# Kernel tuning notes

Hardware: AMD Instinct MI355X
Metric: run time of the kernel (lower is better)

## Reference

```python
import jax, jax.numpy as jnp
import numpy as np

OUT = 4096       # out_features
IN = 4096        # in_features
GS = 128         # group_size
G = IN // GS     # num_groups = 32 (IN divisible by GS -> no padding path)


def setup_inputs() -> dict:
    key = jax.random.key(0)
    k1, k2, k3 = jax.random.split(key, 3)
    x = jax.random.normal(k1, (4096, IN), dtype=jnp.float32)
    # packed int4 weights: each byte holds two 4-bit codes in [0,15] (offset-8)
    qweight = jax.random.randint(k2, (OUT, IN // 2), 0, 256, dtype=jnp.int32)
    # per-(row, group) positive scales
    scale = jax.random.uniform(k3, (OUT, G, 1), dtype=jnp.float32,
                               minval=0.01, maxval=0.1)
    return {"x": x, "qweight": qweight, "scale": scale}


def reference(x, qweight, scale):
    # unpack_int4: high nibble is the even-position element, low nibble odd
    high = (qweight >> 4) & 15
    low = qweight & 15
    q = jnp.stack([high, low], axis=-1).reshape(OUT, -1)  # [OUT, IN]
    q = q.astype(jnp.float32) - 8.0                       # back to [-8, 7]
    # group-wise dequantization
    w = q.reshape(OUT, G, GS) * scale                     # [OUT, G, GS]
    B = x.shape[0]
    xg = x.reshape(B, G, GS)                              # [B, G, GS]
    return jnp.einsum('bgs,ogs->bo', xg, w)               # [B, OUT]
```

## Files before the change

### kernel.cpp

```cpp
#include <hip/hip_runtime.h>

typedef __attribute__((ext_vector_type(8))) _Float16 f16x8;
typedef __attribute__((ext_vector_type(4))) float    f32x4;
typedef __attribute__((ext_vector_type(4))) int      i32x4;

#define IN_F   4096
#define OUT_F  4096
#define NGRP   32
#define NKT    64

#define GLOAD16(gsrc, ldst)                                                   \
    __builtin_amdgcn_global_load_lds(                                         \
        (const __attribute__((address_space(1))) unsigned int*)(gsrc),        \
        (__attribute__((address_space(3))) unsigned int*)(ldst), 16, 0, 0)

#define CFENCE  asm volatile("" ::: "memory")
#define BARRIER do { CFENCE; __builtin_amdgcn_s_barrier(); CFENCE; } while (0)
#define VMW2    asm volatile("s_waitcnt vmcnt(2)" ::: "memory")

__global__ __launch_bounds__(256)
void cvt_x(const float* __restrict__ X, _Float16* __restrict__ Y) {
    size_t i = ((size_t)blockIdx.x * 256 + threadIdx.x) * 8;
    f32x4 a = *(const f32x4*)(X + i);
    f32x4 b = *(const f32x4*)(X + i + 4);
    f16x8 h;
    h[0] = (_Float16)a[0]; h[1] = (_Float16)a[1];
    h[2] = (_Float16)a[2]; h[3] = (_Float16)a[3];
    h[4] = (_Float16)b[0]; h[5] = (_Float16)b[1];
    h[6] = (_Float16)b[2]; h[7] = (_Float16)b[3];
    *(f16x8*)(Y + i) = h;
}

__global__ __launch_bounds__(256)
void deq_w(const int* __restrict__ QW, const float* __restrict__ S,
           _Float16* __restrict__ W) {
    size_t t  = (size_t)blockIdx.x * 256 + threadIdx.x;
    size_t jj = t * 4;
    size_t o  = jj >> 11;
    size_t jr = jj & 2047;
    const float s = S[o * NGRP + (jr >> 6)];
    i32x4 q = *(const i32x4*)(QW + jj);
    f16x8 h;
#pragma unroll
    for (int j = 0; j < 4; ++j) {
        const int v = q[j];
        h[2 * j]     = (_Float16)((float)(((v >> 4) & 15) - 8) * s);
        h[2 * j + 1] = (_Float16)((float)((v & 15) - 8) * s);
    }
    *(f16x8*)(W + jj * 2) = h;
}

__global__ __launch_bounds__(512, 2)
void gemm8p(const _Float16* __restrict__ A,
            const _Float16* __restrict__ B,
            float*          __restrict__ C)
{
    extern __shared__ char LDSc[];
    char* const ldsA = LDSc;
    char* const ldsB = LDSc + 65536;

    const int tid  = threadIdx.x;
    const int lane = tid & 63;
    const int wid  = tid >> 6;
    const int wm   = wid >> 2;
    const int wn   = wid & 3;

    const int bid = blockIdx.x;
    const int swz = (bid & 7) * 32 + (bid >> 3);
    const int bm0 = (swz >> 4) * 256;
    const int bn0 = (swz & 15) * 256;

    const int r0 = tid >> 3;
    const int cs = ((tid & 7) * 16) ^ ((r0 & 7) << 4);
    const _Float16* Asrc = A + (size_t)(bm0 + r0) * IN_F + (cs >> 1);
    const _Float16* Bsrc = B + (size_t)(bn0 + r0) * IN_F + (cs >> 1);
    const int dstoff = wid * 1024;

    const int lane15 = lane & 15;
    const int swr = (lane & 7) << 4;
    const int c0 = ((lane >> 4) * 16) ^ swr;
    const int c1 = (64 + (lane >> 4) * 16) ^ swr;
    int rAoff[4], rBoff[2];
#pragma unroll
    for (int mm = 0; mm < 4; ++mm) rAoff[mm] = (wm * 64 + mm * 16 + lane15) * 128;
#pragma unroll
    for (int nn = 0; nn < 2; ++nn) rBoff[nn] = (wn * 32 + nn * 16 + lane15) * 128;

    f16x8 afr[4][2], blo[2][2], bhi[2][2];
    f32x4 acc[8][4];
#pragma unroll
    for (int m = 0; m < 8; ++m)
#pragma unroll
        for (int n = 0; n < 4; ++n) acc[m][n] = (f32x4)0.0f;

#define STAGE_A(HALF, KT, BUF) do {                                           \
        const _Float16* s_ = Asrc + (size_t)(HALF) * 128 * IN_F + (KT) * 64;  \
        char* d_ = ldsA + ((BUF) * 2 + (HALF)) * 16384 + dstoff;              \
        GLOAD16(s_, d_);                                                      \
        GLOAD16(s_ + (size_t)64 * IN_F, d_ + 8192); } while (0)

#define STAGE_B(HALF, KT, BUF) do {                                           \
        const _Float16* s_ = Bsrc + (size_t)(HALF) * 128 * IN_F + (KT) * 64;  \
        char* d_ = ldsB + ((BUF) * 2 + (HALF)) * 16384 + dstoff;              \
        GLOAD16(s_, d_);                                                      \
        GLOAD16(s_ + (size_t)64 * IN_F, d_ + 8192); } while (0)

#define RD_A(BUF, QM) do { char* ab_ = ldsA + ((BUF) * 2 + (QM)) * 16384;     \
        _Pragma("unroll") for (int mm = 0; mm < 4; ++mm) {                    \
            afr[mm][0] = *(const f16x8*)(ab_ + rAoff[mm] + c0);               \
            afr[mm][1] = *(const f16x8*)(ab_ + rAoff[mm] + c1); } } while (0)

#define RD_B(BUF, QN, DST) do { char* bb_ = ldsB + ((BUF) * 2 + (QN)) * 16384;\
        _Pragma("unroll") for (int nn = 0; nn < 2; ++nn) {                    \
            DST[nn][0] = *(const f16x8*)(bb_ + rBoff[nn] + c0);               \
            DST[nn][1] = *(const f16x8*)(bb_ + rBoff[nn] + c1); } } while (0)

#define MFMA_Q(QM, QN, BQ)                                                    \
        __builtin_amdgcn_s_setprio(1);                                        \
        _Pragma("unroll") for (int mm = 0; mm < 4; ++mm)                      \
        _Pragma("unroll") for (int nn = 0; nn < 2; ++nn)                      \
        _Pragma("unroll") for (int kk = 0; kk < 2; ++kk)                      \
            acc[(QM)*4+mm][(QN)*2+nn] =                                       \
                __builtin_amdgcn_mfma_f32_16x16x32_f16(                       \
                    afr[mm][kk], BQ[nn][kk], acc[(QM)*4+mm][(QN)*2+nn],0,0,0);\
        __builtin_amdgcn_s_setprio(0);

#define GROUP(BUF, NX) do {                                                   \
                                                           \
        VMW2; RD_A(BUF, 0); RD_B(BUF, 0, blo); STAGE_A(0, NX, (BUF) ^ 1);     \
        BARRIER; MFMA_Q(0, 0, blo); BARRIER;                                  \
                                                           \
        VMW2; RD_B(BUF, 1, bhi); STAGE_B(0, NX, (BUF) ^ 1);                   \
        BARRIER; MFMA_Q(0, 1, bhi); BARRIER;                                  \
                                                           \
        RD_A(BUF, 1); STAGE_B(1, NX, (BUF) ^ 1);                              \
        BARRIER; MFMA_Q(1, 0, blo); BARRIER;                                  \
                                                           \
        VMW2; STAGE_A(1, NX, (BUF) ^ 1);                                      \
        BARRIER; MFMA_Q(1, 1, bhi); BARRIER;                                  \
    } while (0)

    STAGE_A(0, 0, 0); STAGE_B(0, 0, 0); STAGE_B(1, 0, 0); STAGE_A(1, 0, 0);
    asm volatile("s_waitcnt vmcnt(4)" ::: "memory");
    BARRIER;

    for (int t = 0; t < NKT; t += 2) {
        GROUP(0, t + 1);
        GROUP(1, (t + 2) & 63);
    }
    asm volatile("s_waitcnt vmcnt(0)" ::: "memory");

#pragma unroll
    for (int m = 0; m < 8; ++m) {
        const int Mr = bm0 + (m >> 2) * 128 + wm * 64 + (m & 3) * 16 + (lane >> 4) * 4;
#pragma unroll
        for (int n = 0; n < 4; ++n) {
            const int Nc = bn0 + (n >> 1) * 128 + wn * 32 + (n & 1) * 16 + lane15;
#pragma unroll
            for (int r = 0; r < 4; ++r)
                C[(size_t)(Mr + r) * OUT_F + Nc] = acc[m][n][r];
        }
    }
#undef STAGE_A
#undef STAGE_B
#undef RD_A
#undef RD_B
#undef MFMA_Q
#undef GROUP
}

__global__ __launch_bounds__(256, 3)
void gemm_f16(const _Float16* __restrict__ A,
              const _Float16* __restrict__ B,
              float*          __restrict__ C)
{
    __shared__ __align__(16) _Float16 lA[128 * 32];
    __shared__ __align__(16) _Float16 lB[128 * 32];

    const int tid  = threadIdx.x;
    const int lane = tid & 63;
    const int bid = blockIdx.x;
    const int swz = (bid & 7) * 128 + (bid >> 3);
    const int bm0 = (swz >> 5) * 128;
    const int bn0 = (swz & 31) * 128;

    const int sr = tid >> 2;
    const int sc = (tid & 3) * 8;
    const _Float16* Aps = A + (size_t)(bm0 + sr) * IN_F + sc;
    const _Float16* Bps = B + (size_t)(bn0 + sr) * IN_F + sc;
    char* lAb = (char*)lA + (tid & ~63) * 16;
    char* lBb = (char*)lB + (tid & ~63) * 16;

    const int wv = tid >> 6;
    const int wr = (wv >> 1) * 64;
    const int wc = (wv & 1)  * 64;
    const int lr  = lane & 15;
    const int lkb = (lane >> 4) * 16;

    f32x4 acc[4][4];
#pragma unroll
    for (int m = 0; m < 4; ++m)
#pragma unroll
        for (int n = 0; n < 4; ++n) acc[m][n] = (f32x4)0.0f;

    for (int kt = 0; kt < 128; ++kt) {
        __syncthreads();
        {
            const _Float16* ak = Aps + kt * 32;
            const _Float16* bk = Bps + kt * 32;
            GLOAD16(ak, lAb);
            GLOAD16(ak + (size_t)64 * IN_F, lAb + 4096);
            GLOAD16(bk, lBb);
            GLOAD16(bk + (size_t)64 * IN_F, lBb + 4096);
        }
        __syncthreads();

        f16x8 a[4], b[4];
#pragma unroll
        for (int m = 0; m < 4; ++m)
            a[m] = *(const f16x8*)((const char*)lA + (wr + m * 16 + lr) * 64 + lkb);
#pragma unroll
        for (int n = 0; n < 4; ++n)
            b[n] = *(const f16x8*)((const char*)lB + (wc + n * 16 + lr) * 64 + lkb);
#pragma unroll
        for (int m = 0; m < 4; ++m)
#pragma unroll
            for (int n = 0; n < 4; ++n)
                acc[m][n] = __builtin_amdgcn_mfma_f32_16x16x32_f16(
                    a[m], b[n], acc[m][n], 0, 0, 0);
    }

    const int crow = bm0 + wr + (lane >> 4) * 4;
    const int ccol = bn0 + wc + lr;
#pragma unroll
    for (int m = 0; m < 4; ++m)
#pragma unroll
        for (int n = 0; n < 4; ++n)
#pragma unroll
            for (int r = 0; r < 4; ++r)
                C[(size_t)(crow + m * 16 + r) * OUT_F + (ccol + n * 16)]
                    = acc[m][n][r];
}

extern "C" void kernel_launch(void* const* d_in, const int* in_sizes, int n_in,
                              void* d_out, int out_size, void* d_ws, size_t ws_size,
                              hipStream_t stream) {
    (void)in_sizes; (void)n_in; (void)out_size; (void)ws_size;
    const float* x  = (const float*)d_in[0];
    const int*   qw = (const int*)d_in[1];
    const float* s  = (const float*)d_in[2];
    float*       out = (float*)d_out;

    _Float16* xf = (_Float16*)d_ws;
    _Float16* wf = xf + (size_t)OUT_F * IN_F;
    cvt_x<<<dim3(8192), dim3(256), 0, stream>>>(x, xf);
    deq_w<<<dim3(8192), dim3(256), 0, stream>>>(qw, s, wf);

    hipError_t e = hipFuncSetAttribute((const void*)gemm8p,
        hipFuncAttributeMaxDynamicSharedMemorySize, 131072);
    if (e == hipSuccess)
        gemm8p<<<dim3(256), dim3(512), 131072, stream>>>(xf, wf, out);
    else
        gemm_f16<<<dim3(1024), dim3(256), 0, stream>>>(xf, wf, out);
}
```

Measured before the change: 142.0 us.

## Deepen global-to-LDS prefetch pipeline with relaxed vmcnt waits

Result: no change. 144.1 us (+1.5%).

```diff
diff --git a/kernel.cpp b/kernel.cpp
--- a/kernel.cpp
+++ b/kernel.cpp
@@ -16,7 +16,7 @@
 
 #define CFENCE  asm volatile("" ::: "memory")
 #define BARRIER do { CFENCE; __builtin_amdgcn_s_barrier(); CFENCE; } while (0)
-#define VMW2    asm volatile("s_waitcnt vmcnt(2)" ::: "memory")
+#define VMW6    asm volatile("s_waitcnt vmcnt(6)" ::: "memory")
 
 __global__ __launch_bounds__(256)
 void cvt_x(const float* __restrict__ X, _Float16* __restrict__ Y) {
@@ -125,28 +125,29 @@
                     afr[mm][kk], BQ[nn][kk], acc[(QM)*4+mm][(QN)*2+nn],0,0,0);\
         __builtin_amdgcn_s_setprio(0);
 
-#define GROUP(BUF, NX) do {                                                   \
-                                                           \
-        VMW2; RD_A(BUF, 0); RD_B(BUF, 0, blo); STAGE_A(0, NX, (BUF) ^ 1);     \
-        BARRIER; MFMA_Q(0, 0, blo); BARRIER;                                  \
-                                                           \
-        VMW2; RD_B(BUF, 1, bhi); STAGE_B(0, NX, (BUF) ^ 1);                   \
-        BARRIER; MFMA_Q(0, 1, bhi); BARRIER;                                  \
-                                                           \
-        RD_A(BUF, 1); STAGE_B(1, NX, (BUF) ^ 1);                              \
-        BARRIER; MFMA_Q(1, 0, blo); BARRIER;                                  \
-                                                           \
-        VMW2; STAGE_A(1, NX, (BUF) ^ 1);                                      \
-        BARRIER; MFMA_Q(1, 1, bhi); BARRIER;                                  \
-    } while (0)
-
     STAGE_A(0, 0, 0); STAGE_B(0, 0, 0); STAGE_B(1, 0, 0); STAGE_A(1, 0, 0);
-    asm volatile("s_waitcnt vmcnt(4)" ::: "memory");
-    BARRIER;
+    STAGE_A(0, 1, 1); STAGE_B(0, 1, 1); STAGE_B(1, 1, 1);
+    VMW6; BARRIER;
 
     for (int t = 0; t < NKT; t += 2) {
-        GROUP(0, t + 1);
-        GROUP(1, (t + 2) & 63);
+        const int k2 = (t + 2) & 63;
+        const int k3 = (t + 3) & 63;
+        RD_A(0, 0); RD_B(0, 0, blo); STAGE_A(1, t + 1, 1);
+        BARRIER; MFMA_Q(0, 0, blo); BARRIER;
+        RD_B(0, 1, bhi); STAGE_A(0, k2, 0);
+        BARRIER; MFMA_Q(0, 1, bhi); BARRIER;
+        RD_A(0, 1); STAGE_B(0, k2, 0);
+        BARRIER; MFMA_Q(1, 0, blo); BARRIER;
+        STAGE_B(1, k2, 0);
+        BARRIER; MFMA_Q(1, 1, bhi); VMW6; BARRIER;
+        RD_A(1, 0); RD_B(1, 0, blo); STAGE_A(1, k2, 0);
+        BARRIER; MFMA_Q(0, 0, blo); BARRIER;
+        RD_B(1, 1, bhi); STAGE_A(0, k3, 1);
+        BARRIER; MFMA_Q(0, 1, bhi); BARRIER;
+        RD_A(1, 1); STAGE_B(0, k3, 1);
+        BARRIER; MFMA_Q(1, 0, blo); BARRIER;
+        STAGE_B(1, k3, 1);
+        BARRIER; MFMA_Q(1, 1, bhi); VMW6; BARRIER;
     }
     asm volatile("s_waitcnt vmcnt(0)" ::: "memory");
 
@@ -166,7 +167,6 @@
 #undef RD_A
 #undef RD_B
 #undef MFMA_Q
-#undef GROUP
 }
 
 __global__ __launch_bounds__(256, 3)
```
